# Kernel optimization log

Measured on AMD Instinct MI355X. Metric: run time of the kernel, lower is better.

The kernel has to match this reference:

```python
import math
import jax, jax.numpy as jnp
import numpy as np

SEQ, IN, HID = 4096, 1024, 1024


def _uniform(key, shape, fan):
    s = 1.0 / math.sqrt(fan)
    return jax.random.uniform(key, shape, jnp.float32, -s, s)


def setup_inputs() -> dict:
    key = jax.random.key(0)
    ks = jax.random.split(key, 16)
    return {
        "x": jax.random.normal(ks[0], (SEQ, 1, IN), jnp.float32),
        "bot_Wih": _uniform(ks[1], (4 * HID, IN), HID),
        "bot_Whh": _uniform(ks[2], (4 * HID, HID), HID),
        "bot_bih": _uniform(ks[3], (4 * HID,), HID),
        "bot_bhh": _uniform(ks[4], (4 * HID,), HID),
        "top_Wih": _uniform(ks[5], (4 * HID, HID), HID),
        "top_Whh": _uniform(ks[6], (4 * HID, HID), HID),
        "top_bih": _uniform(ks[7], (4 * HID,), HID),
        "top_bhh": _uniform(ks[8], (4 * HID,), HID),
        "hw_w": _uniform(ks[9], (HID, HID), HID),
        "hw_b": _uniform(ks[10], (HID,), HID),
        "cw_w": _uniform(ks[11], (HID, HID), HID),
        "cw_b": _uniform(ks[12], (HID,), HID),
        "att_bias": jnp.zeros((HID,), jnp.float32),
        "v2s_w": _uniform(ks[13], (1, HID), HID),
        "v2s_b": _uniform(ks[14], (1,), HID),
    }


def _lstm(xs, Wih, Whh, bih, bhh):
    # xs: (T, D). PyTorch gate order: i, f, g, o. Zero initial state (h_0, c_0).
    H = Whh.shape[1]
    xg = xs @ Wih.T + (bih + bhh)  # (T, 4H) precomputed input projections

    def cell(carry, xg_t):
        h, c = carry
        g = xg_t + h @ Whh.T
        i, f, gg, o = jnp.split(g, 4)
        c = jax.nn.sigmoid(f) * c + jax.nn.sigmoid(i) * jnp.tanh(gg)
        h = jax.nn.sigmoid(o) * jnp.tanh(c)
        return (h, c), h

    z = jnp.zeros((H,), xs.dtype)
    (hT, _), hs = jax.lax.scan(cell, (z, z), xg)
    return hs, hT  # (T, H), (H,)


def reference(x, bot_Wih, bot_Whh, bot_bih, bot_bhh,
              top_Wih, top_Whh, top_bih, top_bhh,
              hw_w, hw_b, cw_w, cw_b, att_bias, v2s_w, v2s_b):
    xs = x[:, 0, :]                      # (T, IN), batch=1 squeezed
    y, _ = _lstm(xs, bot_Wih, bot_Whh, bot_bih, bot_bhh)  # (T, H)

    seq_len = xs.shape[0]
    up_len = min(80, int(math.floor(math.sqrt(seq_len))))
    idx = np.linspace(up_len - 1, up_len ** 2 - 1, num=up_len).astype(np.int64)
    if idx[-1] != seq_len - 1:
        idx = np.concatenate([idx, np.array([seq_len - 1], np.int64)])
    up_x = y[idx]                        # (up_len, H)
    _, ctx = _lstm(up_x, top_Wih, top_Whh, top_bih, top_bhh)  # (H,)

    # ctx is constant over the prefix loop, so per-position logits are i-independent:
    # e_j = v^T tanh(hw(y_j) + cw(ctx) + bias) + v_b
    m = jnp.tanh(y @ hw_w.T + hw_b + (ctx @ cw_w.T + cw_b) + att_bias)  # (T, H)
    e = m @ v2s_w[0] + v2s_b[0]          # (T,)

    # prefix softmax-weighted sums via a single stable cumulative pass
    p = jnp.exp(e - jnp.max(e))          # (T,)
    num = jnp.cumsum(p[:, None] * y, axis=0)  # (T, H)
    den = jnp.cumsum(p)                  # (T,)
    out = num / den[:, None]             # out_i = sum_{j<=i} softmax(e[:i+1])_j * y_j
    return out[:, None, :]               # (T, 1, H)
```

## Files before the change

kernel.cpp:

```cpp
#include <hip/hip_runtime.h>
#include <hip/hip_bf16.h>
#include <cstdint>
#include <cstddef>

#define SEQ 4096
#define HID 1024
#define G4  4096
#define NWG 64
#define TPB 512
#define UPL 64

__device__ float    g_xg[(size_t)SEQ * G4];
__device__ float    g_y [(size_t)SEQ * HID];
__device__ float    g_h [2][HID];
__device__ float    g_h2[2][HID];
__device__ float    g_upx[(size_t)UPL * HID];
__device__ float    g_bias2[HID];
__device__ float    g_e[SEQ];
__device__ float    g_p[SEQ];
__device__ float    g_invden[SEQ];
__device__ float    g_csum[64 * HID];
__device__ unsigned g_bar;

__global__ void k_init() { g_bar = 0u; }

__device__ __forceinline__ float atomLoad(float* p) {
  return __hip_atomic_load(p, __ATOMIC_RELAXED, __HIP_MEMORY_SCOPE_AGENT);
}
__device__ __forceinline__ void atomStore(float* p, float v) {
  __hip_atomic_store(p, v, __ATOMIC_RELAXED, __HIP_MEMORY_SCOPE_AGENT);
}

#define BMT 128
#define BNT 128
#define BKT 32

__global__ __launch_bounds__(256) void k_gemm_xg(const float* __restrict__ A,
                                                 const float* __restrict__ B,
                                                 const float* __restrict__ bias0,
                                                 const float* __restrict__ bias1)
{
  __shared__ float As[BKT][BMT + 4];
  __shared__ float Bs[BKT][BNT + 4];
  const int t  = threadIdx.x;
  const int bn = blockIdx.x;
  const int bm = blockIdx.y;
  const int m0 = (t & 15) * 8;
  const int n0 = (t >> 4) * 8;

  float acc[8][8];
#pragma unroll
  for (int i = 0; i < 8; i++)
#pragma unroll
    for (int j = 0; j < 8; j++) acc[i][j] = 0.f;

  for (int k0 = 0; k0 < 1024; k0 += BKT) {
#pragma unroll
    for (int i = 0; i < 4; i++) {
      const int idx = i * 256 + t;
      const int m   = idx >> 3;
      const int k4  = (idx & 7) << 2;
      const float4 av = *(const float4*)&A[(size_t)(bm * BMT + m) * 1024 + k0 + k4];
      As[k4 + 0][m] = av.x; As[k4 + 1][m] = av.y; As[k4 + 2][m] = av.z; As[k4 + 3][m] = av.w;
      const float4 bv = *(const float4*)&B[(size_t)(bn * BNT + m) * 1024 + k0 + k4];
      Bs[k4 + 0][m] = bv.x; Bs[k4 + 1][m] = bv.y; Bs[k4 + 2][m] = bv.z; Bs[k4 + 3][m] = bv.w;
    }
    __syncthreads();
#pragma unroll
    for (int k = 0; k < BKT; k++) {
      float a[8], b[8];
      *(float4*)&a[0] = *(const float4*)&As[k][m0];
      *(float4*)&a[4] = *(const float4*)&As[k][m0 + 4];
      *(float4*)&b[0] = *(const float4*)&Bs[k][n0];
      *(float4*)&b[4] = *(const float4*)&Bs[k][n0 + 4];
#pragma unroll
      for (int i = 0; i < 8; i++)
#pragma unroll
        for (int j = 0; j < 8; j++) acc[i][j] = fmaf(a[i], b[j], acc[i][j]);
    }
    __syncthreads();
  }

  float bb[8];
#pragma unroll
  for (int j = 0; j < 8; j++) {
    const int gc = bn * BNT + n0 + j;
    bb[j] = bias0[gc] + bias1[gc];
  }
#pragma unroll
  for (int i = 0; i < 8; i++) {
    const size_t off = (size_t)(bm * BMT + m0 + i) * G4 + bn * BNT + n0;
    float4 v0, v1;
    v0.x = acc[i][0] + bb[0]; v0.y = acc[i][1] + bb[1]; v0.z = acc[i][2] + bb[2]; v0.w = acc[i][3] + bb[3];
    v1.x = acc[i][4] + bb[4]; v1.y = acc[i][5] + bb[5]; v1.z = acc[i][6] + bb[6]; v1.w = acc[i][7] + bb[7];
    *(float4*)&g_xg[off]     = v0;
    *(float4*)&g_xg[off + 4] = v1;
  }
}

__device__ __forceinline__ void grid_sync(unsigned target)
{
  asm volatile("s_waitcnt vmcnt(0)" ::: "memory");
  __syncthreads();
  if (threadIdx.x == 0) {
    __hip_atomic_fetch_add(&g_bar, 1u, __ATOMIC_RELAXED, __HIP_MEMORY_SCOPE_AGENT);
    while (__hip_atomic_load(&g_bar, __ATOMIC_RELAXED, __HIP_MEMORY_SCOPE_AGENT) < target) { }
  }
  __syncthreads();
  asm volatile("" ::: "memory");
}

__device__ __forceinline__ float seg_dot32(const float4* __restrict__ wv,
                                           const float* __restrict__ hb, int seg)
{
  float acc = 0.f;
#pragma unroll
  for (int k = 0; k < 32; k++) {
    const float4 hv = *(const float4*)&hb[((k + seg) & 31) << 2];
    acc = fmaf(wv[k].x, hv.x, acc);
    acc = fmaf(wv[k].y, hv.y, acc);
    acc = fmaf(wv[k].z, hv.z, acc);
    acc = fmaf(wv[k].w, hv.w, acc);
  }
  return acc;
}

__device__ __forceinline__ void load_wrow(float4* __restrict__ wv,
                                          const float* __restrict__ W, int row, int seg)
{
  const float* wr = W + (size_t)row * HID + (seg << 7);
#pragma unroll
  for (int k = 0; k < 32; k++) wv[k] = *(const float4*)&wr[((k + seg) & 31) << 2];
}

__global__ __launch_bounds__(TPB, 2) void k_lstm(
    const float* __restrict__ bot_Whh,
    const float* __restrict__ top_Wih, const float* __restrict__ top_Whh,
    const float* __restrict__ top_bih, const float* __restrict__ top_bhh,
    const float* __restrict__ hw_b,    const float* __restrict__ cw_w,
    const float* __restrict__ cw_b,    const float* __restrict__ att_bias)
{
  const int w = blockIdx.x;
  const int t = threadIdx.x;
  const int r_local = t >> 3;
  const int seg     = t & 7;
  const int row = ((r_local >> 4) << 10) + (w << 4) + (r_local & 15);

  __shared__ float h_lds[HID];
  __shared__ float gates_lds[64];
  __shared__ float xg2_lds[UPL][64];

  float4 wv[32];
  load_wrow(wv, bot_Whh, row, seg);

  float c_state = 0.f;
  unsigned gen = 0;
  const int i0 = t << 1;

  for (int step = 0; step < SEQ; step++) {
    float xval = 0.f;
    if (seg == 0) xval = g_xg[(size_t)step * G4 + row];
    if (step == 0) {
      for (int i = t; i < HID; i += TPB) h_lds[i] = 0.f;
    } else {
      float* src = g_h[(step + 1) & 1];
      h_lds[i0]     = atomLoad(&src[i0]);
      h_lds[i0 + 1] = atomLoad(&src[i0 + 1]);
    }
    __syncthreads();
    float acc = seg_dot32(wv, &h_lds[seg << 7], seg);
    acc += __shfl_xor(acc, 4);
    acc += __shfl_xor(acc, 2);
    acc += __shfl_xor(acc, 1);
    if (seg == 0) gates_lds[r_local] = acc + xval;
    __syncthreads();
    if (t < 16) {
      const float gi = gates_lds[t];
      const float gf = gates_lds[16 + t];
      const float gg = gates_lds[32 + t];
      const float go = gates_lds[48 + t];
      const float ii = 1.f / (1.f + expf(-gi));
      const float ff = 1.f / (1.f + expf(-gf));
      c_state = ff * c_state + ii * tanhf(gg);
      const float hh = (1.f / (1.f + expf(-go))) * tanhf(c_state);
      atomStore(&g_h[step & 1][(w << 4) + t], hh);
      g_y[(size_t)step * HID + (w << 4) + t] = hh;
      if ((step & 63) == 63)
        atomStore(&g_upx[(size_t)(step >> 6) * HID + (w << 4) + t], hh);
    }
    ++gen;
    grid_sync(gen * NWG);
  }

  load_wrow(wv, top_Wih, row, seg);
  const float tb = top_bih[row] + top_bhh[row];
  for (int s = 0; s < UPL; s++) {
    __syncthreads();
    {
      float* src = &g_upx[(size_t)s * HID];
      h_lds[i0]     = atomLoad(&src[i0]);
      h_lds[i0 + 1] = atomLoad(&src[i0 + 1]);
    }
    __syncthreads();
    float acc = seg_dot32(wv, &h_lds[seg << 7], seg);
    acc += __shfl_xor(acc, 4);
    acc += __shfl_xor(acc, 2);
    acc += __shfl_xor(acc, 1);
    if (seg == 0) xg2_lds[s][r_local] = acc + tb;
  }

  load_wrow(wv, top_Whh, row, seg);
  c_state = 0.f;
  for (int s = 0; s < UPL; s++) {
    if (s == 0) {
      __syncthreads();
      for (int i = t; i < HID; i += TPB) h_lds[i] = 0.f;
    } else {
      float* src = g_h2[(s + 1) & 1];
      h_lds[i0]     = atomLoad(&src[i0]);
      h_lds[i0 + 1] = atomLoad(&src[i0 + 1]);
    }
    __syncthreads();
    float acc = seg_dot32(wv, &h_lds[seg << 7], seg);
    acc += __shfl_xor(acc, 4);
    acc += __shfl_xor(acc, 2);
    acc += __shfl_xor(acc, 1);
    if (seg == 0) gates_lds[r_local] = acc + xg2_lds[s][r_local];
    __syncthreads();
    if (t < 16) {
      const float gi = gates_lds[t];
      const float gf = gates_lds[16 + t];
      const float gg = gates_lds[32 + t];
      const float go = gates_lds[48 + t];
      const float ii = 1.f / (1.f + expf(-gi));
      const float ff = 1.f / (1.f + expf(-gf));
      c_state = ff * c_state + ii * tanhf(gg);
      const float hh = (1.f / (1.f + expf(-go))) * tanhf(c_state);
      atomStore(&g_h2[s & 1][(w << 4) + t], hh);
    }
    ++gen;
    grid_sync(gen * NWG);
  }

  __syncthreads();
  {
    float* src = g_h2[1];
    h_lds[i0]     = atomLoad(&src[i0]);
    h_lds[i0 + 1] = atomLoad(&src[i0 + 1]);
  }
  __syncthreads();
  {
    const int jl = t >> 5;
    const int ks = t & 31;
    const int j  = (w << 4) + jl;
    const float* cr = cw_w + (size_t)j * HID + (ks << 5);
    const float* hr = &h_lds[ks << 5];
    float a2 = 0.f;
#pragma unroll
    for (int k = 0; k < 32; k++) a2 = fmaf(cr[k], hr[k], a2);
    a2 += __shfl_xor(a2, 16);
    a2 += __shfl_xor(a2, 8);
    a2 += __shfl_xor(a2, 4);
    a2 += __shfl_xor(a2, 2);
    a2 += __shfl_xor(a2, 1);
    if (ks == 0) g_bias2[j] = a2 + hw_b[j] + cw_b[j] + att_bias[j];
  }
}

__global__ __launch_bounds__(256) void k_attn_e(const float* __restrict__ hw_w,
                                                const float* __restrict__ v2s_w,
                                                const float* __restrict__ v2s_b)
{
  __shared__ float ys[16][1028];
  __shared__ float ws[16][1028];
  const int b  = blockIdx.x;
  const int t  = threadIdx.x;
  const int rg = t >> 6;
  const int fg = (t >> 4) & 3;
  const int ks = t & 15;

#pragma unroll
  for (int i = 0; i < 16; i++) {
    const int idx = i * 256 + t;
    const int r   = idx >> 8;
    const int c4  = (idx & 255) << 2;
    *(float4*)&ys[r][c4] = *(const float4*)&g_y[(size_t)((b << 4) + r) * HID + c4];
  }

  float e_acc[4] = {0.f, 0.f, 0.f, 0.f};
  for (int f0 = 0; f0 < HID; f0 += 16) {
    __syncthreads();
#pragma unroll
    for (int i = 0; i < 16; i++) {
      const int idx = i * 256 + t;
      const int r   = idx >> 8;
      const int c4  = (idx & 255) << 2;
      *(float4*)&ws[r][c4] = *(const float4*)&hw_w[(size_t)(f0 + r) * HID + c4];
    }
    __syncthreads();

    float acc[4][4];
#pragma unroll
    for (int u = 0; u < 4; u++)
#pragma unroll
      for (int v = 0; v < 4; v++) acc[u][v] = 0.f;

#pragma unroll
    for (int m = 0; m < 16; m++) {
      const int k4 = (ks << 6) + (((m + ks) & 15) << 2);
      float4 av[4], bv[4];
#pragma unroll
      for (int u = 0; u < 4; u++) av[u] = *(const float4*)&ys[(rg << 2) + u][k4];
#pragma unroll
      for (int v = 0; v < 4; v++) bv[v] = *(const float4*)&ws[(fg << 2) + v][k4];
#pragma unroll
      for (int u = 0; u < 4; u++)
#pragma unroll
        for (int v = 0; v < 4; v++) {
          acc[u][v] = fmaf(av[u].x, bv[v].x, acc[u][v]);
          acc[u][v] = fmaf(av[u].y, bv[v].y, acc[u][v]);
          acc[u][v] = fmaf(av[u].z, bv[v].z, acc[u][v]);
          acc[u][v] = fmaf(av[u].w, bv[v].w, acc[u][v]);
        }
    }
#pragma unroll
    for (int u = 0; u < 4; u++)
#pragma unroll
      for (int v = 0; v < 4; v++) {
        float s2 = acc[u][v];
        s2 += __shfl_xor(s2, 8);
        s2 += __shfl_xor(s2, 4);
        s2 += __shfl_xor(s2, 2);
        s2 += __shfl_xor(s2, 1);
        acc[u][v] = s2;
      }
    if (ks == 0) {
#pragma unroll
      for (int v = 0; v < 4; v++) {
        const int j = f0 + (fg << 2) + v;
        const float bias = g_bias2[j];
        const float vw   = v2s_w[j];
#pragma unroll
        for (int u = 0; u < 4; u++)
          e_acc[u] += vw * tanhf(acc[u][v] + bias);
      }
    }
  }
#pragma unroll
  for (int u = 0; u < 4; u++) {
    float s2 = e_acc[u];
    s2 += __shfl_xor(s2, 16);
    s2 += __shfl_xor(s2, 32);
    if (fg == 0 && ks == 0) g_e[(b << 4) + (rg << 2) + u] = s2 + v2s_b[0];
  }
}

__global__ __launch_bounds__(1024) void k_softmax()
{
  const int t  = threadIdx.x;
  const int ln = t & 63;
  const int wv = t >> 6;
  __shared__ float sred[16];
  __shared__ float soff[16];
  __shared__ float sM;

  const float4 ev = *(const float4*)&g_e[t << 2];
  float mx = fmaxf(fmaxf(ev.x, ev.y), fmaxf(ev.z, ev.w));
#pragma unroll
  for (int d = 32; d >= 1; d >>= 1) mx = fmaxf(mx, __shfl_xor(mx, d));
  if (ln == 0) sred[wv] = mx;
  __syncthreads();
  if (t == 0) {
    float m2 = sred[0];
    for (int i = 1; i < 16; i++) m2 = fmaxf(m2, sred[i]);
    sM = m2;
  }
  __syncthreads();
  const float M = sM;
  float4 pv;
  pv.x = expf(ev.x - M); pv.y = expf(ev.y - M); pv.z = expf(ev.z - M); pv.w = expf(ev.w - M);
  *(float4*)&g_p[t << 2] = pv;

  const float s = pv.x + pv.y + pv.z + pv.w;
  float ps = s;
#pragma unroll
  for (int d = 1; d < 64; d <<= 1) {
    const float v = __shfl_up(ps, d);
    if (ln >= d) ps += v;
  }
  __syncthreads();
  if (ln == 63) sred[wv] = ps;
  __syncthreads();
  if (t == 0) {
    float r = 0.f;
    for (int i = 0; i < 16; i++) { soff[i] = r; r += sred[i]; }
  }
  __syncthreads();
  const float base = soff[wv] + (ps - s);
  const float d0 = base + pv.x;
  const float d1 = d0 + pv.y;
  const float d2 = d1 + pv.z;
  const float d3 = d2 + pv.w;
  float4 iv;
  iv.x = 1.f / d0; iv.y = 1.f / d1; iv.z = 1.f / d2; iv.w = 1.f / d3;
  *(float4*)&g_invden[t << 2] = iv;
}

__global__ __launch_bounds__(256) void k_csum()
{
  const int ch = blockIdx.x;
  const int t  = threadIdx.x;
  float ax = 0.f, ay = 0.f, az = 0.f, aw = 0.f;
  for (int r = 0; r < 64; r++) {
    const int row = (ch << 6) + r;
    const float pr = g_p[row];
    const float4 yv = *(const float4*)&g_y[(size_t)row * HID + (t << 2)];
    ax = fmaf(pr, yv.x, ax); ay = fmaf(pr, yv.y, ay);
    az = fmaf(pr, yv.z, az); aw = fmaf(pr, yv.w, aw);
  }
  float4 o; o.x = ax; o.y = ay; o.z = az; o.w = aw;
  *(float4*)&g_csum[(ch << 10) + (t << 2)] = o;
}

__global__ __launch_bounds__(256) void k_cscan()
{
  const int c = blockIdx.x * 256 + threadIdx.x;
  float run = 0.f;
  for (int ch = 0; ch < 64; ch++) {
    const float v = g_csum[(ch << 10) + c];
    g_csum[(ch << 10) + c] = run;
    run += v;
  }
}

__global__ __launch_bounds__(256) void k_final(float* __restrict__ out)
{
  const int ch = blockIdx.x;
  const int t  = threadIdx.x;
  float4 run = *(const float4*)&g_csum[(ch << 10) + (t << 2)];
  for (int r = 0; r < 64; r++) {
    const int row = (ch << 6) + r;
    const float pr = g_p[row];
    const float iv = g_invden[row];
    const float4 yv = *(const float4*)&g_y[(size_t)row * HID + (t << 2)];
    run.x = fmaf(pr, yv.x, run.x);
    run.y = fmaf(pr, yv.y, run.y);
    run.z = fmaf(pr, yv.z, run.z);
    run.w = fmaf(pr, yv.w, run.w);
    float4 ov;
    ov.x = run.x * iv; ov.y = run.y * iv; ov.z = run.z * iv; ov.w = run.w * iv;
    *(float4*)&out[(size_t)row * HID + (t << 2)] = ov;
  }
}

extern "C" void kernel_launch(void* const* d_in, const int* in_sizes, int n_in,
                              void* d_out, int out_size, void* d_ws, size_t ws_size,
                              hipStream_t stream)
{
  (void)in_sizes; (void)n_in; (void)d_ws; (void)ws_size; (void)out_size;

  const float* x        = (const float*)d_in[0];
  const float* bot_Wih  = (const float*)d_in[1];
  const float* bot_Whh  = (const float*)d_in[2];
  const float* bot_bih  = (const float*)d_in[3];
  const float* bot_bhh  = (const float*)d_in[4];
  const float* top_Wih  = (const float*)d_in[5];
  const float* top_Whh  = (const float*)d_in[6];
  const float* top_bih  = (const float*)d_in[7];
  const float* top_bhh  = (const float*)d_in[8];
  const float* hw_w     = (const float*)d_in[9];
  const float* hw_b     = (const float*)d_in[10];
  const float* cw_w     = (const float*)d_in[11];
  const float* cw_b     = (const float*)d_in[12];
  const float* att_bias = (const float*)d_in[13];
  const float* v2s_w    = (const float*)d_in[14];
  const float* v2s_b    = (const float*)d_in[15];
  float* out = (float*)d_out;

  k_init<<<dim3(1), dim3(1), 0, stream>>>();
  k_gemm_xg<<<dim3(32, 32), dim3(256), 0, stream>>>(x, bot_Wih, bot_bih, bot_bhh);
  k_lstm<<<dim3(NWG), dim3(TPB), 0, stream>>>(bot_Whh, top_Wih, top_Whh,
                                              top_bih, top_bhh,
                                              hw_b, cw_w, cw_b, att_bias);
  k_attn_e<<<dim3(256), dim3(256), 0, stream>>>(hw_w, v2s_w, v2s_b);
  k_softmax<<<dim3(1), dim3(1024), 0, stream>>>();
  k_csum<<<dim3(64), dim3(256), 0, stream>>>();
  k_cscan<<<dim3(4), dim3(256), 0, stream>>>();
  k_final<<<dim3(64), dim3(256), 0, stream>>>(out);
}
```

Before: 14.47 ms.

## Replace grid barrier with tagged per-element h flags and spread LSTM over more blocks

The persistent LSTM kernel drops the global atomic-counter grid barrier. Each hidden value is now published as a 64-bit word packing the value with a step tag, and consumers spin on each element until its tag matches. The kernel doubles the workgroup count so each wavefront owns one hidden unit's four gate rows. Gate math moves into a wavefront via shuffles, removing an LDS round trip and a __syncthreads per step. The intent is to cut per-step synchronisation latency on the serial recurrence. The cost is more spinning traffic on global memory and double-buffered LDS, and correctness relies on tags with buffers cleared by k_init.

```diff
diff --git a/kernel.cpp b/kernel.cpp
--- a/kernel.cpp
+++ b/kernel.cpp
@@ -6,29 +6,41 @@
 #define SEQ 4096
 #define HID 1024
 #define G4  4096
-#define NWG 64
+#define NWG 128
 #define TPB 512
 #define UPL 64
 
-__device__ float    g_xg[(size_t)SEQ * G4];
-__device__ float    g_y [(size_t)SEQ * HID];
-__device__ float    g_h [2][HID];
-__device__ float    g_h2[2][HID];
-__device__ float    g_upx[(size_t)UPL * HID];
-__device__ float    g_bias2[HID];
-__device__ float    g_e[SEQ];
-__device__ float    g_p[SEQ];
-__device__ float    g_invden[SEQ];
-__device__ float    g_csum[64 * HID];
-__device__ unsigned g_bar;
-
-__global__ void k_init() { g_bar = 0u; }
-
-__device__ __forceinline__ float atomLoad(float* p) {
+typedef unsigned long long u64;
+
+__device__ float g_xg[(size_t)SEQ * G4];
+__device__ float g_y [(size_t)SEQ * HID];
+__device__ u64   g_hp [2][HID];
+__device__ u64   g_h2p[2][HID];
+__device__ u64   g_upxp[(size_t)UPL * HID];
+__device__ float g_bias2[HID];
+__device__ float g_e[SEQ];
+__device__ float g_p[SEQ];
+__device__ float g_invden[SEQ];
+__device__ float g_csum[64 * HID];
+
+__global__ __launch_bounds__(256) void k_init()
+{
+  const int i = blockIdx.x * 256 + threadIdx.x;
+  if (i < 2 * HID) {
+    ((u64*)g_hp)[i]  = 0ull;
+    ((u64*)g_h2p)[i] = 0ull;
+  }
+  for (int k = i; k < UPL * HID; k += gridDim.x * 256) g_upxp[k] = 0ull;
+}
+
+__device__ __forceinline__ u64 atomLoad64(const u64* p) {
   return __hip_atomic_load(p, __ATOMIC_RELAXED, __HIP_MEMORY_SCOPE_AGENT);
 }
-__device__ __forceinline__ void atomStore(float* p, float v) {
+__device__ __forceinline__ void atomStore64(u64* p, u64 v) {
   __hip_atomic_store(p, v, __ATOMIC_RELAXED, __HIP_MEMORY_SCOPE_AGENT);
+}
+__device__ __forceinline__ u64 packPair(float v, unsigned tag) {
+  return ((u64)tag << 32) | (u64)__float_as_uint(v);
 }
 
 #define BMT 128
@@ -98,39 +110,29 @@
   }
 }
 
-__device__ __forceinline__ void grid_sync(unsigned target)
-{
-  asm volatile("s_waitcnt vmcnt(0)" ::: "memory");
-  __syncthreads();
-  if (threadIdx.x == 0) {
-    __hip_atomic_fetch_add(&g_bar, 1u, __ATOMIC_RELAXED, __HIP_MEMORY_SCOPE_AGENT);
-    while (__hip_atomic_load(&g_bar, __ATOMIC_RELAXED, __HIP_MEMORY_SCOPE_AGENT) < target) { }
-  }
-  __syncthreads();
-  asm volatile("" ::: "memory");
-}
-
-__device__ __forceinline__ float seg_dot32(const float4* __restrict__ wv,
-                                           const float* __restrict__ hb, int seg)
+
+__device__ __forceinline__ void load_w16(float4* __restrict__ wv,
+                                         const float* __restrict__ W,
+                                         int row, int j)
+{
+  const float* wr = W + (size_t)row * HID + (j << 6);
+#pragma unroll
+  for (int k = 0; k < 16; k++) wv[k] = *(const float4*)&wr[((k + j) & 15) << 2];
+}
+
+__device__ __forceinline__ float dot16(const float4* __restrict__ wv,
+                                       const float* __restrict__ hb, int j)
 {
   float acc = 0.f;
 #pragma unroll
-  for (int k = 0; k < 32; k++) {
-    const float4 hv = *(const float4*)&hb[((k + seg) & 31) << 2];
+  for (int k = 0; k < 16; k++) {
+    const float4 hv = *(const float4*)&hb[((k + j) & 15) << 2];
     acc = fmaf(wv[k].x, hv.x, acc);
     acc = fmaf(wv[k].y, hv.y, acc);
     acc = fmaf(wv[k].z, hv.z, acc);
     acc = fmaf(wv[k].w, hv.w, acc);
   }
   return acc;
-}
-
-__device__ __forceinline__ void load_wrow(float4* __restrict__ wv,
-                                          const float* __restrict__ W, int row, int seg)
-{
-  const float* wr = W + (size_t)row * HID + (seg << 7);
-#pragma unroll
-  for (int k = 0; k < 32; k++) wv[k] = *(const float4*)&wr[((k + seg) & 31) << 2];
 }
 
 __global__ __launch_bounds__(TPB, 2) void k_lstm(
@@ -140,130 +142,160 @@
     const float* __restrict__ hw_b,    const float* __restrict__ cw_w,
     const float* __restrict__ cw_b,    const float* __restrict__ att_bias)
 {
-  const int w = blockIdx.x;
-  const int t = threadIdx.x;
-  const int r_local = t >> 3;
-  const int seg     = t & 7;
-  const int row = ((r_local >> 4) << 10) + (w << 4) + (r_local & 15);
-
-  __shared__ float h_lds[HID];
-  __shared__ float gates_lds[64];
-  __shared__ float xg2_lds[UPL][64];
-
-  float4 wv[32];
-  load_wrow(wv, bot_Whh, row, seg);
+  const int w  = blockIdx.x;
+  const int t  = threadIdx.x;
+  const int q  = t >> 6;
+  const int l  = t & 63;
+  const int g  = l >> 4;
+  const int j  = l & 15;
+  const int u  = (w << 3) + q;
+  const int row = (g << 10) + u;
+  const int i0 = t << 1;
+
+  __shared__ float hl[2][HID];
+  __shared__ float xg2_lds[UPL][32];
+
+  float4 wv[16];
+  load_w16(wv, bot_Whh, row, j);
 
   float c_state = 0.f;
-  unsigned gen = 0;
-  const int i0 = t << 1;
 
   for (int step = 0; step < SEQ; step++) {
     float xval = 0.f;
-    if (seg == 0) xval = g_xg[(size_t)step * G4 + row];
+    if (j == 0) xval = g_xg[(size_t)step * G4 + row];
+
+    float* hc = hl[step & 1];
     if (step == 0) {
-      for (int i = t; i < HID; i += TPB) h_lds[i] = 0.f;
+      hc[i0] = 0.f; hc[i0 + 1] = 0.f;
     } else {
-      float* src = g_h[(step + 1) & 1];
-      h_lds[i0]     = atomLoad(&src[i0]);
-      h_lds[i0 + 1] = atomLoad(&src[i0 + 1]);
-    }
-    __syncthreads();
-    float acc = seg_dot32(wv, &h_lds[seg << 7], seg);
+      const u64* src = g_hp[(step + 1) & 1];
+      const unsigned tg = (unsigned)step;
+      u64 v0 = atomLoad64(&src[i0]);
+      u64 v1 = atomLoad64(&src[i0 + 1]);
+      while ((unsigned)(v0 >> 32) != tg) v0 = atomLoad64(&src[i0]);
+      while ((unsigned)(v1 >> 32) != tg) v1 = atomLoad64(&src[i0 + 1]);
+      hc[i0]     = __uint_as_float((unsigned)v0);
+      hc[i0 + 1] = __uint_as_float((unsigned)v1);
+    }
+    __syncthreads();
+
+    float acc = dot16(wv, &hc[j << 6], j);
+    acc += __shfl_xor(acc, 1);
+    acc += __shfl_xor(acc, 2);
     acc += __shfl_xor(acc, 4);
+    acc += __shfl_xor(acc, 8);
+    acc += xval;
+
+    const float gi = __shfl(acc, 0);
+    const float gf = __shfl(acc, 16);
+    const float gg = __shfl(acc, 32);
+    const float go = __shfl(acc, 48);
+    const float ii = 1.f / (1.f + expf(-gi));
+    const float ff = 1.f / (1.f + expf(-gf));
+    c_state = ff * c_state + ii * tanhf(gg);
+    const float hh = (1.f / (1.f + expf(-go))) * tanhf(c_state);
+
+    if (l == 0) {
+      atomStore64(&g_hp[step & 1][u], packPair(hh, (unsigned)(step + 1)));
+      g_y[(size_t)step * HID + u] = hh;
+      if ((step & 63) == 63)
+        atomStore64(&g_upxp[((size_t)(step >> 6) << 10) + u],
+                    packPair(hh, (unsigned)((step >> 6) + 1)));
+    }
+  }
+
+  load_w16(wv, top_Wih, row, j);
+  float tb = 0.f;
+  if (j == 0) tb = top_bih[row] + top_bhh[row];
+  for (int s = 0; s < UPL; s++) {
+    float* hc = hl[s & 1];
+    {
+      const u64* src = &g_upxp[(size_t)s << 10];
+      const unsigned tg = (unsigned)(s + 1);
+      u64 v0 = atomLoad64(&src[i0]);
+      u64 v1 = atomLoad64(&src[i0 + 1]);
+      while ((unsigned)(v0 >> 32) != tg) v0 = atomLoad64(&src[i0]);
+      while ((unsigned)(v1 >> 32) != tg) v1 = atomLoad64(&src[i0 + 1]);
+      hc[i0]     = __uint_as_float((unsigned)v0);
+      hc[i0 + 1] = __uint_as_float((unsigned)v1);
+    }
+    __syncthreads();
+    float acc = dot16(wv, &hc[j << 6], j);
+    acc += __shfl_xor(acc, 1);
     acc += __shfl_xor(acc, 2);
-    acc += __shfl_xor(acc, 1);
-    if (seg == 0) gates_lds[r_local] = acc + xval;
-    __syncthreads();
-    if (t < 16) {
-      const float gi = gates_lds[t];
-      const float gf = gates_lds[16 + t];
-      const float gg = gates_lds[32 + t];
-      const float go = gates_lds[48 + t];
-      const float ii = 1.f / (1.f + expf(-gi));
-      const float ff = 1.f / (1.f + expf(-gf));
-      c_state = ff * c_state + ii * tanhf(gg);
-      const float hh = (1.f / (1.f + expf(-go))) * tanhf(c_state);
-      atomStore(&g_h[step & 1][(w << 4) + t], hh);
-      g_y[(size_t)step * HID + (w << 4) + t] = hh;
-      if ((step & 63) == 63)
-        atomStore(&g_upx[(size_t)(step >> 6) * HID + (w << 4) + t], hh);
-    }
-    ++gen;
-    grid_sync(gen * NWG);
-  }
-
-  load_wrow(wv, top_Wih, row, seg);
-  const float tb = top_bih[row] + top_bhh[row];
-  for (int s = 0; s < UPL; s++) {
-    __syncthreads();
-    {
-      float* src = &g_upx[(size_t)s * HID];
-      h_lds[i0]     = atomLoad(&src[i0]);
-      h_lds[i0 + 1] = atomLoad(&src[i0 + 1]);
-    }
-    __syncthreads();
-    float acc = seg_dot32(wv, &h_lds[seg << 7], seg);
     acc += __shfl_xor(acc, 4);
-    acc += __shfl_xor(acc, 2);
-    acc += __shfl_xor(acc, 1);
-    if (seg == 0) xg2_lds[s][r_local] = acc + tb;
-  }
-
-  load_wrow(wv, top_Whh, row, seg);
+    acc += __shfl_xor(acc, 8);
+    if (j == 0) xg2_lds[s][(q << 2) + g] = acc + tb;
+  }
+
+  load_w16(wv, top_Whh, row, j);
   c_state = 0.f;
   for (int s = 0; s < UPL; s++) {
+    float* hc = hl[s & 1];
     if (s == 0) {
-      __syncthreads();
-      for (int i = t; i < HID; i += TPB) h_lds[i] = 0.f;
+      hc[i0] = 0.f; hc[i0 + 1] = 0.f;
     } else {
-      float* src = g_h2[(s + 1) & 1];
-      h_lds[i0]     = atomLoad(&src[i0]);
-      h_lds[i0 + 1] = atomLoad(&src[i0 + 1]);
-    }
-    __syncthreads();
-    float acc = seg_dot32(wv, &h_lds[seg << 7], seg);
+      const u64* src = g_h2p[(s + 1) & 1];
+      const unsigned tg = (unsigned)s;
+      u64 v0 = atomLoad64(&src[i0]);
+      u64 v1 = atomLoad64(&src[i0 + 1]);
+      while ((unsigned)(v0 >> 32) != tg) v0 = atomLoad64(&src[i0]);
+      while ((unsigned)(v1 >> 32) != tg) v1 = atomLoad64(&src[i0 + 1]);
+      hc[i0]     = __uint_as_float((unsigned)v0);
+      hc[i0 + 1] = __uint_as_float((unsigned)v1);
+    }
+    __syncthreads();
+    float acc = dot16(wv, &hc[j << 6], j);
+    acc += __shfl_xor(acc, 1);
+    acc += __shfl_xor(acc, 2);
     acc += __shfl_xor(acc, 4);
-    acc += __shfl_xor(acc, 2);
-    acc += __shfl_xor(acc, 1);
-    if (seg == 0) gates_lds[r_local] = acc + xg2_lds[s][r_local];
-    __syncthreads();
-    if (t < 16) {
-      const float gi = gates_lds[t];
-      const float gf = gates_lds[16 + t];
-      const float gg = gates_lds[32 + t];
-      const float go = gates_lds[48 + t];
-      const float ii = 1.f / (1.f + expf(-gi));
-      const float ff = 1.f / (1.f + expf(-gf));
-      c_state = ff * c_state + ii * tanhf(gg);
-      const float hh = (1.f / (1.f + expf(-go))) * tanhf(c_state);
-      atomStore(&g_h2[s & 1][(w << 4) + t], hh);
-    }
-    ++gen;
-    grid_sync(gen * NWG);
-  }
-
-  __syncthreads();
+    acc += __shfl_xor(acc, 8);
+    acc += xg2_lds[s][(q << 2) + g];
+
+    const float gi = __shfl(acc, 0);
+    const float gf = __shfl(acc, 16);
+    const float gg = __shfl(acc, 32);
+    const float go = __shfl(acc, 48);
+    const float ii = 1.f / (1.f + expf(-gi));
+    const float ff = 1.f / (1.f + expf(-gf));
+    c_state = ff * c_state + ii * tanhf(gg);
+    const float hh = (1.f / (1.f + expf(-go))) * tanhf(c_state);
+
+    if (l == 0)
+      atomStore64(&g_h2p[s & 1][u], packPair(hh, (unsigned)(s + 1)));
+  }
+
   {
-    float* src = g_h2[1];
-    h_lds[i0]     = atomLoad(&src[i0]);
-    h_lds[i0 + 1] = atomLoad(&src[i0 + 1]);
-  }
-  __syncthreads();
-  {
-    const int jl = t >> 5;
-    const int ks = t & 31;
-    const int j  = (w << 4) + jl;
-    const float* cr = cw_w + (size_t)j * HID + (ks << 5);
-    const float* hr = &h_lds[ks << 5];
+    float* hc = hl[0];
+    const u64* src = g_h2p[1];
+    const unsigned tg = (unsigned)UPL;
+    u64 v0 = atomLoad64(&src[i0]);
+    u64 v1 = atomLoad64(&src[i0 + 1]);
+    while ((unsigned)(v0 >> 32) != tg) v0 = atomLoad64(&src[i0]);
+    while ((unsigned)(v1 >> 32) != tg) v1 = atomLoad64(&src[i0 + 1]);
+    hc[i0]     = __uint_as_float((unsigned)v0);
+    hc[i0 + 1] = __uint_as_float((unsigned)v1);
+    __syncthreads();
+
+    const float* cr = cw_w + (size_t)u * HID + (l << 4);
+    const float* hr = &hc[l << 4];
     float a2 = 0.f;
 #pragma unroll
-    for (int k = 0; k < 32; k++) a2 = fmaf(cr[k], hr[k], a2);
+    for (int k4 = 0; k4 < 4; k4++) {
+      const float4 cv = *(const float4*)&cr[k4 << 2];
+      const float4 hv = *(const float4*)&hr[k4 << 2];
+      a2 = fmaf(cv.x, hv.x, a2);
+      a2 = fmaf(cv.y, hv.y, a2);
+      a2 = fmaf(cv.z, hv.z, a2);
+      a2 = fmaf(cv.w, hv.w, a2);
+    }
+    a2 += __shfl_xor(a2, 1);
+    a2 += __shfl_xor(a2, 2);
+    a2 += __shfl_xor(a2, 4);
+    a2 += __shfl_xor(a2, 8);
     a2 += __shfl_xor(a2, 16);
-    a2 += __shfl_xor(a2, 8);
-    a2 += __shfl_xor(a2, 4);
-    a2 += __shfl_xor(a2, 2);
-    a2 += __shfl_xor(a2, 1);
-    if (ks == 0) g_bias2[j] = a2 + hw_b[j] + cw_b[j] + att_bias[j];
+    a2 += __shfl_xor(a2, 32);
+    if (l == 0) g_bias2[u] = a2 + hw_b[u] + cw_b[u] + att_bias[u];
   }
 }
 
@@ -337,9 +369,9 @@
     if (ks == 0) {
 #pragma unroll
       for (int v = 0; v < 4; v++) {
-        const int j = f0 + (fg << 2) + v;
-        const float bias = g_bias2[j];
-        const float vw   = v2s_w[j];
+        const int jj = f0 + (fg << 2) + v;
+        const float bias = g_bias2[jj];
+        const float vw   = v2s_w[jj];
 #pragma unroll
         for (int u = 0; u < 4; u++)
           e_acc[u] += vw * tanhf(acc[u][v] + bias);
@@ -477,7 +509,7 @@
   const float* v2s_b    = (const float*)d_in[15];
   float* out = (float*)d_out;
 
-  k_init<<<dim3(1), dim3(1), 0, stream>>>();
+  k_init<<<dim3(64), dim3(256), 0, stream>>>();
   k_gemm_xg<<<dim3(32, 32), dim3(256), 0, stream>>>(x, bot_Wih, bot_bih, bot_bhh);
   k_lstm<<<dim3(NWG), dim3(TPB), 0, stream>>>(bot_Whh, top_Wih, top_Whh,
                                               top_bih, top_bhh,
```

Measured after the change: 18.70 ms, median of 4. 29.2% more time.
